# Kernel tuning notes

Measured on AMD Instinct MI355X. Metric: run time of the kernel, lower is better.

Reference implementation:

```python
import jax, jax.numpy as jnp
import numpy as np


def _build_masks():
    # pathways_mask: [G genes, P pathways], K genes per pathway (deterministic)
    G, P, K = 5000, 200, 100
    rng = np.random.default_rng(0)
    r = rng.random((G, P))
    pm = np.zeros((G, P), np.float32)
    pm[np.argpartition(r, K, axis=0)[:K], np.arange(P)[None, :]] = 1.0
    l1 = np.maximum(pm.sum(0).astype(np.int64) // 5, 4)   # divide_nodes/min_nodes defaults
    l2 = np.maximum(l1 // 2, 3)
    l3 = np.maximum(l2 // 2, 2)
    g1 = np.repeat(np.arange(P), l1)
    g2 = np.repeat(np.arange(P), l2)
    g3 = np.repeat(np.arange(P), l3)
    # masks stored transposed, [out_features, in_features], as in MaskedLinear buffer
    m1 = np.repeat(pm, l1, axis=1).T                                  # [H1, G]
    m2 = (g2[:, None] == g1[None, :]).astype(np.float32)              # [H2, H1] block-diag repeated
    m3 = (g3[:, None] == g2[None, :]).astype(np.float32)              # [H3, H2]
    m4 = (np.arange(P)[:, None] == g3[None, :]).astype(np.float32)    # [P,  H3] final_mask
    return m1, m2, m3, m4


def setup_inputs():
    B, NL = 8192, 50
    m1, m2, m3, m4 = _build_masks()
    dims = [m1.shape[1], m1.shape[0], m2.shape[0], m3.shape[0], m4.shape[0]]  # [5000,4000,2000,1000,200]
    key = jax.random.key(0)
    ks = iter(jax.random.split(key, 40))
    def W(o, i):
        return jax.random.normal(next(ks), (o, i), jnp.float32) / np.sqrt(i)
    def V(n):
        return jax.random.normal(next(ks), (n,), jnp.float32) * 0.1
    inp = {"x": jax.random.normal(next(ks), (B, dims[0]), jnp.float32)}
    for li, (i, o, m) in enumerate(zip(dims[:4], dims[1:], [m1, m2, m3, m4]), 1):
        inp[f"w{li}"] = W(o, i)
        inp[f"b{li}"] = V(o)
        inp[f"m{li}"] = jnp.asarray(m)
    for li, o in enumerate(dims[1:4], 1):
        inp[f"gamma{li}"] = 1.0 + V(o)
        inp[f"beta{li}"] = V(o)
        inp[f"rm{li}"] = V(o)
        inp[f"rv{li}"] = 0.5 + jax.random.uniform(next(ks), (o,), jnp.float32)
    inp["wc"] = W(NL, dims[4])
    inp["bc"] = V(NL)
    return inp


def _bn_relu(h, gamma, beta, rm, rv):
    # eval-mode BatchNorm1d (running stats) + ReLU; Dropout is identity at eval
    return jax.nn.relu(gamma * (h - rm) * jax.lax.rsqrt(rv + 1e-5) + beta)


def reference(x, w1, b1, m1, w2, b2, m2, w3, b3, m3, w4, b4, m4,
              gamma1, beta1, rm1, rv1, gamma2, beta2, rm2, rv2,
              gamma3, beta3, rm3, rv3, wc, bc):
    h = _bn_relu(x @ (w1 * m1).T + b1, gamma1, beta1, rm1, rv1)
    h = _bn_relu(h @ (w2 * m2).T + b2, gamma2, beta2, rm2, rv2)
    h = _bn_relu(h @ (w3 * m3).T + b3, gamma3, beta3, rm3, rv3)
    scores = jax.nn.relu(h @ (w4 * m4).T + b4)   # [B, n_pathways]
    return scores @ wc.T + bc                    # [B, n_labels]
```

## Files before the change

### kernel.cpp

```cpp
#include <hip/hip_runtime.h>
#include <hip/hip_fp16.h>
#include <stdint.h>

#define GENES 5000
#define NH1   4000
#define NH2   2000
#define NH3   1000
#define NPATH 200
#define NLAB  50
#define NROWS 8192
#define KP    100

typedef _Float16 f16x2 __attribute__((ext_vector_type(2)));
union H2U { unsigned int u; f16x2 v; __half2 h; };

__device__ __forceinline__ float dot2acc(unsigned int a, unsigned int b, float c){
#if __has_builtin(__builtin_amdgcn_fdot2)
    H2U ua; ua.u = a; H2U ub; ub.u = b;
    return __builtin_amdgcn_fdot2(ua.v, ub.v, c, false);
#else
    H2U ua; ua.u = a; H2U ub; ub.u = b;
    float2 fa = __half22float2(ua.h), fb = __half22float2(ub.h);
    return fmaf(fa.x, fb.x, fmaf(fa.y, fb.y, c));
#endif
}

__device__ __forceinline__ unsigned pklo(unsigned xa, unsigned xb){
#if __has_builtin(__builtin_amdgcn_perm)
    return __builtin_amdgcn_perm(xb, xa, 0x05040100u);
#else
    return (xa & 0xffffu) | (xb << 16);
#endif
}
__device__ __forceinline__ unsigned pkhi(unsigned xa, unsigned xb){
#if __has_builtin(__builtin_amdgcn_perm)
    return __builtin_amdgcn_perm(xb, xa, 0x07060302u);
#else
    return (xa >> 16) | (xb & 0xffff0000u);
#endif
}

__global__ void k_idx(const float* __restrict__ m1, int* __restrict__ idx1){
    __shared__ int cnt;
    if (threadIdx.x == 0) cnt = 0;
    __syncthreads();
    const float* row = m1 + (size_t)blockIdx.x * 20 * GENES;
    for (int g = threadIdx.x; g < GENES; g += blockDim.x){
        if (row[g] != 0.0f){
            int pos = atomicAdd(&cnt, 1);
            if (pos < KP) idx1[blockIdx.x * KP + pos] = g;
        }
    }
}

__global__ void k_wg1(const float* __restrict__ w1, const float* __restrict__ gamma1,
                      const float* __restrict__ rv1, const int* __restrict__ idx1,
                      __half* __restrict__ wg1p){
    int tid = blockIdx.x * 256 + threadIdx.x;
    if (tid >= 400000) return;
    int kk  = tid / 8000;
    int rem = tid % 8000;
    int c = rem >> 3;
    int e = rem & 7;
    int p = c / 5, g = c % 5;
    int u = e >> 1, kpar = e & 1;
    int k = kk * 2 + kpar;
    int j = p * 20 + g * 4 + u;
    int col = idx1[p * KP + k];
    float a = gamma1[j] * rsqrtf(rv1[j] + 1e-5f);
    wg1p[tid] = (__half)(w1[(size_t)j * GENES + col] * a);
}

__global__ void k_prep(const float* __restrict__ w2, const float* __restrict__ b2,
                       const float* __restrict__ w3, const float* __restrict__ b3,
                       const float* __restrict__ w4, const float* __restrict__ wc,
                       const float* __restrict__ gamma1, const float* __restrict__ beta1,
                       const float* __restrict__ rm1, const float* __restrict__ rv1,
                       const float* __restrict__ gamma2, const float* __restrict__ beta2,
                       const float* __restrict__ rm2, const float* __restrict__ rv2,
                       const float* __restrict__ gamma3, const float* __restrict__ beta3,
                       const float* __restrict__ rm3, const float* __restrict__ rv3,
                       const float* __restrict__ b1,
                       float* __restrict__ bf1, float* __restrict__ bf2,
                       float* __restrict__ bf3,
                       __half* __restrict__ wpk, float* __restrict__ wcT){
    int t = blockIdx.x * 256 + threadIdx.x;
    if (t < 40000){
        int p = t / 200, i = t % 200;
        int u2 = i / 20, k = i % 20;
        int j = 10 * p + u2;
        float a = gamma2[j] * rsqrtf(rv2[j] + 1e-5f);
        wpk[p * 256 + i] = (__half)(w2[(size_t)j * NH1 + 20 * p + k] * a);
    } else if (t < 50000){
        int i2 = t - 40000;
        int p = i2 / 50, i = i2 % 50;
        int u3 = i / 10, k = i % 10;
        int j = 5 * p + u3;
        float a = gamma3[j] * rsqrtf(rv3[j] + 1e-5f);
        wpk[p * 256 + 200 + i] = (__half)(w3[(size_t)j * NH2 + 10 * p + k] * a);
    } else if (t < 51000){
        int i2 = t - 50000;
        int p = i2 / 5, k = i2 % 5;
        wpk[p * 256 + 250 + k] = (__half)(w4[(size_t)p * NH3 + 5 * p + k]);
    } else if (t < 51200){
        int p = t - 51000;
        wpk[p * 256 + 255] = (__half)0.0f;
    } else if (t < 61200){
        int i = t - 51200;
        int q = i / NLAB, n = i % NLAB;
        wcT[i] = wc[(size_t)n * NPATH + q];
    } else if (t < 65200){
        int j = t - 61200;
        float a = gamma1[j] * rsqrtf(rv1[j] + 1e-5f);
        bf1[j] = a * b1[j] + beta1[j] - rm1[j] * a;
    } else if (t < 67200){
        int j = t - 65200;
        float a = gamma2[j] * rsqrtf(rv2[j] + 1e-5f);
        bf2[j] = a * b2[j] + beta2[j] - rm2[j] * a;
    } else if (t < 68200){
        int j = t - 67200;
        float a = gamma3[j] * rsqrtf(rv3[j] + 1e-5f);
        bf3[j] = a * b3[j] + beta3[j] - rm3[j] * a;
    }
}

__global__ __launch_bounds__(256) void k_layer1(const float* __restrict__ x,
        const int* __restrict__ idx1, const __half* __restrict__ wg1p,
        const float* __restrict__ bf1, __half* __restrict__ h1buf){
    __shared__ __align__(16) __half xs[GENES * 4];
    const int r0 = blockIdx.x * 4;
    for (int c = threadIdx.x; c < GENES; c += 256){
        float v0 = x[(size_t)(r0 + 0) * GENES + c];
        float v1 = x[(size_t)(r0 + 1) * GENES + c];
        float v2 = x[(size_t)(r0 + 2) * GENES + c];
        float v3 = x[(size_t)(r0 + 3) * GENES + c];
        __half2* d = (__half2*)(xs + c * 4);
        d[0] = __floats2half2_rn(v0, v1);
        d[1] = __floats2half2_rn(v2, v3);
    }
    __syncthreads();
    const int t = threadIdx.x;
    if (t >= 250) return;
    const int pl = t / 5, g = t % 5;
    for (int pass = 0; pass < 4; ++pass){
        const int p = pass * 50 + pl;
        float acc[4][4];
        #pragma unroll
        for (int u = 0; u < 4; ++u)
            #pragma unroll
            for (int r = 0; r < 4; ++r) acc[u][r] = 0.0f;
        const int2* ip = (const int2*)(idx1 + p * KP);
        const char* wb = (const char*)(((const uint4*)wg1p) + (p * 5 + g));
        int2 ivA = ip[0], ivB = ip[1];
        uint4 wvA = *(const uint4*)wb;
        uint4 wvB = *(const uint4*)(wb + 16000);
        for (int kk = 0; kk < 50; kk += 2){
            const int nk = (kk + 2 < 50) ? kk + 2 : 0;
            int2 ivA2 = ip[nk], ivB2 = ip[nk + 1];
            uint4 wvA2 = *(const uint4*)(wb + (size_t)nk * 16000);
            uint4 wvB2 = *(const uint4*)(wb + (size_t)(nk + 1) * 16000);
            {
                uint2 xa = *(const uint2*)(xs + ivA.x * 4);
                uint2 xb = *(const uint2*)(xs + ivA.y * 4);
                unsigned pr[4] = { pklo(xa.x, xb.x), pkhi(xa.x, xb.x),
                                   pklo(xa.y, xb.y), pkhi(xa.y, xb.y) };
                const unsigned wu[4] = {wvA.x, wvA.y, wvA.z, wvA.w};
                #pragma unroll
                for (int u = 0; u < 4; ++u)
                    #pragma unroll
                    for (int r = 0; r < 4; ++r)
                        acc[u][r] = dot2acc(pr[r], wu[u], acc[u][r]);
            }
            {
                uint2 xa = *(const uint2*)(xs + ivB.x * 4);
                uint2 xb = *(const uint2*)(xs + ivB.y * 4);
                unsigned pr[4] = { pklo(xa.x, xb.x), pkhi(xa.x, xb.x),
                                   pklo(xa.y, xb.y), pkhi(xa.y, xb.y) };
                const unsigned wu[4] = {wvB.x, wvB.y, wvB.z, wvB.w};
                #pragma unroll
                for (int u = 0; u < 4; ++u)
                    #pragma unroll
                    for (int r = 0; r < 4; ++r)
                        acc[u][r] = dot2acc(pr[r], wu[u], acc[u][r]);
            }
            ivA = ivA2; ivB = ivB2; wvA = wvA2; wvB = wvB2;
        }
        const float4 bf = ((const float4*)bf1)[p * 5 + g];
        const float bfa[4] = {bf.x, bf.y, bf.z, bf.w};
        const int jb = p * 20 + g * 4;
        #pragma unroll
        for (int r = 0; r < 4; ++r){
            __half2 o01 = __floats2half2_rn(fmaxf(acc[0][r] + bfa[0], 0.0f),
                                            fmaxf(acc[1][r] + bfa[1], 0.0f));
            __half2 o23 = __floats2half2_rn(fmaxf(acc[2][r] + bfa[2], 0.0f),
                                            fmaxf(acc[3][r] + bfa[3], 0.0f));
            uint2 st; st.x = *(unsigned*)&o01; st.y = *(unsigned*)&o23;
            *(uint2*)(h1buf + (size_t)(r0 + r) * NH1 + jb) = st;
        }
    }
}

__global__ __launch_bounds__(256) void k_tail(const __half* __restrict__ h1buf,
        const __half* __restrict__ wpk, const float* __restrict__ bf2,
        const float* __restrict__ bf3, const float* __restrict__ b4,
        const float* __restrict__ wcT, const float* __restrict__ bc,
        float* __restrict__ out){
    __shared__ float scs[8 * NPATH];
    __shared__ __align__(16) float wcs[NPATH * NLAB];
    const int t = threadIdx.x;
    const int r0 = blockIdx.x * 8;
    for (int i = t; i < (NPATH * NLAB) / 4; i += 256)
        ((float4*)wcs)[i] = ((const float4*)wcT)[i];
    if (t < NPATH){
        const int p = t;
        unsigned cw[128];
        const uint4* wp4 = (const uint4*)(wpk + p * 256);
        #pragma unroll
        for (int i = 0; i < 32; ++i){
            uint4 v = wp4[i];
            cw[4*i] = v.x; cw[4*i+1] = v.y; cw[4*i+2] = v.z; cw[4*i+3] = v.w;
        }
        float c2[10], c3[5];
        #pragma unroll
        for (int i = 0; i < 10; ++i) c2[i] = bf2[10 * p + i];
        #pragma unroll
        for (int i = 0; i < 5; ++i)  c3[i] = bf3[5 * p + i];
        const float b4p = b4[p];
        for (int r = 0; r < 8; ++r){
            const uint2* hp = (const uint2*)(h1buf + (size_t)(r0 + r) * NH1 + 20 * p);
            unsigned h1u[10];
            #pragma unroll
            for (int i = 0; i < 5; ++i){ uint2 v = hp[i]; h1u[2*i] = v.x; h1u[2*i+1] = v.y; }
            unsigned h2u[5];
            #pragma unroll
            for (int i = 0; i < 5; ++i){
                float a0 = c2[2*i], a1 = c2[2*i+1];
                #pragma unroll
                for (int kk = 0; kk < 10; ++kk){
                    a0 = dot2acc(h1u[kk], cw[(2*i) * 10 + kk], a0);
                    a1 = dot2acc(h1u[kk], cw[(2*i+1) * 10 + kk], a1);
                }
                __half2 hh = __floats2half2_rn(fmaxf(a0, 0.f), fmaxf(a1, 0.f));
                h2u[i] = *(unsigned*)&hh;
            }
            float h3f[5];
            #pragma unroll
            for (int u = 0; u < 5; ++u){
                float a = c3[u];
                #pragma unroll
                for (int kk = 0; kk < 5; ++kk)
                    a = dot2acc(h2u[kk], cw[100 + u * 5 + kk], a);
                h3f[u] = fmaxf(a, 0.f);
            }
            unsigned h3u[3];
            __half2 t01 = __floats2half2_rn(h3f[0], h3f[1]); h3u[0] = *(unsigned*)&t01;
            __half2 t23 = __floats2half2_rn(h3f[2], h3f[3]); h3u[1] = *(unsigned*)&t23;
            __half2 t4  = __floats2half2_rn(h3f[4], 0.f);    h3u[2] = *(unsigned*)&t4;
            float a = b4p;
            #pragma unroll
            for (int kk = 0; kk < 3; ++kk)
                a = dot2acc(h3u[kk], cw[125 + kk], a);
            scs[r * NPATH + p] = fmaxf(a, 0.f);
        }
    }
    __syncthreads();
    for (int o = t; o < 8 * NLAB; o += 256){
        int r = o / NLAB, n = o % NLAB;
        float acc = bc[n];
        const float* sp = scs + r * NPATH;
        #pragma unroll 8
        for (int q = 0; q < NPATH; ++q)
            acc = fmaf(sp[q], wcs[q * NLAB + n], acc);
        out[(size_t)(r0 + r) * NLAB + n] = acc;
    }
}

extern "C" void kernel_launch(void* const* d_in, const int* in_sizes, int n_in,
                              void* d_out, int out_size, void* d_ws, size_t ws_size,
                              hipStream_t stream){
    (void)in_sizes; (void)n_in; (void)out_size; (void)ws_size;
    const float* x      = (const float*)d_in[0];
    const float* w1     = (const float*)d_in[1];
    const float* b1     = (const float*)d_in[2];
    const float* m1     = (const float*)d_in[3];
    const float* w2     = (const float*)d_in[4];
    const float* b2     = (const float*)d_in[5];
    const float* w3     = (const float*)d_in[7];
    const float* b3     = (const float*)d_in[8];
    const float* w4     = (const float*)d_in[10];
    const float* b4     = (const float*)d_in[11];
    const float* gamma1 = (const float*)d_in[13];
    const float* beta1  = (const float*)d_in[14];
    const float* rm1    = (const float*)d_in[15];
    const float* rv1    = (const float*)d_in[16];
    const float* gamma2 = (const float*)d_in[17];
    const float* beta2  = (const float*)d_in[18];
    const float* rm2    = (const float*)d_in[19];
    const float* rv2    = (const float*)d_in[20];
    const float* gamma3 = (const float*)d_in[21];
    const float* beta3  = (const float*)d_in[22];
    const float* rm3    = (const float*)d_in[23];
    const float* rv3    = (const float*)d_in[24];
    const float* wc     = (const float*)d_in[25];
    const float* bc     = (const float*)d_in[26];

    char* ws = (char*)d_ws;
    size_t off = 0;
    __half* h1buf = (__half*)(ws + off); off += (size_t)NROWS * NH1 * 2;
    int*    idx1  = (int*)  (ws + off);  off += (size_t)NPATH * KP * 4;
    __half* wg1p  = (__half*)(ws + off); off += (size_t)400000 * 2;
    float*  bf1   = (float*)(ws + off);  off += (size_t)NH1 * 4;
    float*  bf2   = (float*)(ws + off);  off += (size_t)NH2 * 4;
    float*  bf3   = (float*)(ws + off);  off += (size_t)NH3 * 4;
    __half* wpk   = (__half*)(ws + off); off += (size_t)NPATH * 256 * 2;
    float*  wcT   = (float*)(ws + off);  off += (size_t)NPATH * NLAB * 4;

    hipLaunchKernelGGL(k_idx,    dim3(NPATH),   dim3(256), 0, stream, m1, idx1);
    hipLaunchKernelGGL(k_wg1,    dim3(1563),    dim3(256), 0, stream, w1, gamma1, rv1, idx1, wg1p);
    hipLaunchKernelGGL(k_prep,   dim3(267),     dim3(256), 0, stream,
                       w2, b2, w3, b3, w4, wc,
                       gamma1, beta1, rm1, rv1, gamma2, beta2, rm2, rv2,
                       gamma3, beta3, rm3, rv3, b1,
                       bf1, bf2, bf3, wpk, wcT);
    hipLaunchKernelGGL(k_layer1, dim3(NROWS/4), dim3(256), 0, stream, x, idx1, wg1p, bf1, h1buf);
    hipLaunchKernelGGL(k_tail,   dim3(NROWS/8), dim3(256), 0, stream,
                       h1buf, wpk, bf2, bf3, b4, wcT, bc, (float*)d_out);
}
```

Before: 538.6 us.

## Fuse layer1 and tail kernels, keep h1 in shared memory, 6 rows per block

Merges the layer-1 sparse gather kernel and the tail kernel into a single kernel that keeps the h1 activations in registers and then shared memory, so the 8192x4000 half-precision h1 buffer is never written to or read back from global memory. Each block now handles 6 rows instead of 4 and uses a deeper software-pipelined gather loop. The two weight-prep kernels are merged into one launch. The final classifier now reads wcT from global memory instead of staging it in shared memory. The trade-off is heavier register pressure (48 h1 registers plus 24 accumulators per thread), about 60KB of shared memory per block, and a row count that does not divide evenly into blocks, which adds a tail guard.

```diff
diff --git a/kernel.cpp b/kernel.cpp
--- a/kernel.cpp
+++ b/kernel.cpp
@@ -10,6 +10,7 @@
 #define NLAB  50
 #define NROWS 8192
 #define KP    100
+#define RB    6
 
 typedef _Float16 f16x2 __attribute__((ext_vector_type(2)));
 union H2U { unsigned int u; f16x2 v; __half2 h; };
@@ -53,38 +54,38 @@
     }
 }
 
-__global__ void k_wg1(const float* __restrict__ w1, const float* __restrict__ gamma1,
-                      const float* __restrict__ rv1, const int* __restrict__ idx1,
-                      __half* __restrict__ wg1p){
-    int tid = blockIdx.x * 256 + threadIdx.x;
-    if (tid >= 400000) return;
-    int kk  = tid / 8000;
-    int rem = tid % 8000;
-    int c = rem >> 3;
-    int e = rem & 7;
-    int p = c / 5, g = c % 5;
-    int u = e >> 1, kpar = e & 1;
-    int k = kk * 2 + kpar;
-    int j = p * 20 + g * 4 + u;
-    int col = idx1[p * KP + k];
-    float a = gamma1[j] * rsqrtf(rv1[j] + 1e-5f);
-    wg1p[tid] = (__half)(w1[(size_t)j * GENES + col] * a);
-}
-
-__global__ void k_prep(const float* __restrict__ w2, const float* __restrict__ b2,
-                       const float* __restrict__ w3, const float* __restrict__ b3,
-                       const float* __restrict__ w4, const float* __restrict__ wc,
-                       const float* __restrict__ gamma1, const float* __restrict__ beta1,
-                       const float* __restrict__ rm1, const float* __restrict__ rv1,
-                       const float* __restrict__ gamma2, const float* __restrict__ beta2,
-                       const float* __restrict__ rm2, const float* __restrict__ rv2,
-                       const float* __restrict__ gamma3, const float* __restrict__ beta3,
-                       const float* __restrict__ rm3, const float* __restrict__ rv3,
-                       const float* __restrict__ b1,
-                       float* __restrict__ bf1, float* __restrict__ bf2,
-                       float* __restrict__ bf3,
-                       __half* __restrict__ wpk, float* __restrict__ wcT){
-    int t = blockIdx.x * 256 + threadIdx.x;
+__global__ void k_prep2(const float* __restrict__ w1, const float* __restrict__ gamma1,
+                        const float* __restrict__ rv1, const int* __restrict__ idx1,
+                        __half* __restrict__ wg1p,
+                        const float* __restrict__ w2, const float* __restrict__ b2,
+                        const float* __restrict__ w3, const float* __restrict__ b3,
+                        const float* __restrict__ w4, const float* __restrict__ wc,
+                        const float* __restrict__ beta1, const float* __restrict__ rm1,
+                        const float* __restrict__ gamma2, const float* __restrict__ beta2,
+                        const float* __restrict__ rm2, const float* __restrict__ rv2,
+                        const float* __restrict__ gamma3, const float* __restrict__ beta3,
+                        const float* __restrict__ rm3, const float* __restrict__ rv3,
+                        const float* __restrict__ b1,
+                        float* __restrict__ bf1, float* __restrict__ bf2,
+                        float* __restrict__ bf3,
+                        __half* __restrict__ wpk, float* __restrict__ wcT){
+    if (blockIdx.x < 1563){
+        int tid = blockIdx.x * 256 + threadIdx.x;
+        if (tid >= 400000) return;
+        int kk  = tid / 8000;
+        int rem = tid % 8000;
+        int c = rem >> 3;
+        int e = rem & 7;
+        int p = c / 5, g = c % 5;
+        int u = e >> 1, kpar = e & 1;
+        int k = kk * 2 + kpar;
+        int j = p * 20 + g * 4 + u;
+        int col = idx1[p * KP + k];
+        float a = gamma1[j] * rsqrtf(rv1[j] + 1e-5f);
+        wg1p[tid] = (__half)(w1[(size_t)j * GENES + col] * a);
+        return;
+    }
+    int t = (blockIdx.x - 1563) * 256 + threadIdx.x;
     if (t < 40000){
         int p = t / 200, i = t % 200;
         int u2 = i / 20, k = i % 20;
@@ -124,93 +125,94 @@
     }
 }
 
-__global__ __launch_bounds__(256) void k_layer1(const float* __restrict__ x,
+__global__ __launch_bounds__(256, 2) void k_main(const float* __restrict__ x,
         const int* __restrict__ idx1, const __half* __restrict__ wg1p,
-        const float* __restrict__ bf1, __half* __restrict__ h1buf){
-    __shared__ __align__(16) __half xs[GENES * 4];
-    const int r0 = blockIdx.x * 4;
-    for (int c = threadIdx.x; c < GENES; c += 256){
-        float v0 = x[(size_t)(r0 + 0) * GENES + c];
-        float v1 = x[(size_t)(r0 + 1) * GENES + c];
-        float v2 = x[(size_t)(r0 + 2) * GENES + c];
-        float v3 = x[(size_t)(r0 + 3) * GENES + c];
-        __half2* d = (__half2*)(xs + c * 4);
-        d[0] = __floats2half2_rn(v0, v1);
-        d[1] = __floats2half2_rn(v2, v3);
-    }
-    __syncthreads();
-    const int t = threadIdx.x;
-    if (t >= 250) return;
-    const int pl = t / 5, g = t % 5;
-    for (int pass = 0; pass < 4; ++pass){
-        const int p = pass * 50 + pl;
-        float acc[4][4];
-        #pragma unroll
-        for (int u = 0; u < 4; ++u)
-            #pragma unroll
-            for (int r = 0; r < 4; ++r) acc[u][r] = 0.0f;
-        const int2* ip = (const int2*)(idx1 + p * KP);
-        const char* wb = (const char*)(((const uint4*)wg1p) + (p * 5 + g));
-        int2 ivA = ip[0], ivB = ip[1];
-        uint4 wvA = *(const uint4*)wb;
-        uint4 wvB = *(const uint4*)(wb + 16000);
-        for (int kk = 0; kk < 50; kk += 2){
-            const int nk = (kk + 2 < 50) ? kk + 2 : 0;
-            int2 ivA2 = ip[nk], ivB2 = ip[nk + 1];
-            uint4 wvA2 = *(const uint4*)(wb + (size_t)nk * 16000);
-            uint4 wvB2 = *(const uint4*)(wb + (size_t)(nk + 1) * 16000);
-            {
-                uint2 xa = *(const uint2*)(xs + ivA.x * 4);
-                uint2 xb = *(const uint2*)(xs + ivA.y * 4);
-                unsigned pr[4] = { pklo(xa.x, xb.x), pkhi(xa.x, xb.x),
-                                   pklo(xa.y, xb.y), pkhi(xa.y, xb.y) };
-                const unsigned wu[4] = {wvA.x, wvA.y, wvA.z, wvA.w};
-                #pragma unroll
-                for (int u = 0; u < 4; ++u)
-                    #pragma unroll
-                    for (int r = 0; r < 4; ++r)
-                        acc[u][r] = dot2acc(pr[r], wu[u], acc[u][r]);
-            }
-            {
-                uint2 xa = *(const uint2*)(xs + ivB.x * 4);
-                uint2 xb = *(const uint2*)(xs + ivB.y * 4);
-                unsigned pr[4] = { pklo(xa.x, xb.x), pkhi(xa.x, xb.x),
-                                   pklo(xa.y, xb.y), pkhi(xa.y, xb.y) };
-                const unsigned wu[4] = {wvB.x, wvB.y, wvB.z, wvB.w};
-                #pragma unroll
-                for (int u = 0; u < 4; ++u)
-                    #pragma unroll
-                    for (int r = 0; r < 4; ++r)
-                        acc[u][r] = dot2acc(pr[r], wu[u], acc[u][r]);
-            }
-            ivA = ivA2; ivB = ivB2; wvA = wvA2; wvB = wvB2;
-        }
-        const float4 bf = ((const float4*)bf1)[p * 5 + g];
-        const float bfa[4] = {bf.x, bf.y, bf.z, bf.w};
-        const int jb = p * 20 + g * 4;
-        #pragma unroll
-        for (int r = 0; r < 4; ++r){
-            __half2 o01 = __floats2half2_rn(fmaxf(acc[0][r] + bfa[0], 0.0f),
-                                            fmaxf(acc[1][r] + bfa[1], 0.0f));
-            __half2 o23 = __floats2half2_rn(fmaxf(acc[2][r] + bfa[2], 0.0f),
-                                            fmaxf(acc[3][r] + bfa[3], 0.0f));
-            uint2 st; st.x = *(unsigned*)&o01; st.y = *(unsigned*)&o23;
-            *(uint2*)(h1buf + (size_t)(r0 + r) * NH1 + jb) = st;
-        }
-    }
-}
-
-__global__ __launch_bounds__(256) void k_tail(const __half* __restrict__ h1buf,
+        const float* __restrict__ bf1,
         const __half* __restrict__ wpk, const float* __restrict__ bf2,
         const float* __restrict__ bf3, const float* __restrict__ b4,
         const float* __restrict__ wcT, const float* __restrict__ bc,
         float* __restrict__ out){
-    __shared__ float scs[8 * NPATH];
-    __shared__ __align__(16) float wcs[NPATH * NLAB];
+    __shared__ __align__(16) unsigned char smem[60000];
+    __shared__ float scs[RB * NPATH];
     const int t = threadIdx.x;
-    const int r0 = blockIdx.x * 8;
-    for (int i = t; i < (NPATH * NLAB) / 4; i += 256)
-        ((float4*)wcs)[i] = ((const float4*)wcT)[i];
+    const int r0 = blockIdx.x * RB;
+    const int rvld = min(RB, NROWS - r0);
+
+    for (int c = t; c < GENES; c += 256){
+        float v[RB];
+        #pragma unroll
+        for (int r = 0; r < RB; ++r)
+            v[r] = (r < rvld) ? x[(size_t)(r0 + r) * GENES + c] : 0.0f;
+        unsigned* d = (unsigned*)(smem + c * 12);
+        __half2 h01 = __floats2half2_rn(v[0], v[1]);
+        __half2 h23 = __floats2half2_rn(v[2], v[3]);
+        __half2 h45 = __floats2half2_rn(v[4], v[5]);
+        d[0] = *(unsigned*)&h01; d[1] = *(unsigned*)&h23; d[2] = *(unsigned*)&h45;
+    }
+    __syncthreads();
+
+    unsigned h1r[48];
+    const int pl = t / 5, g = t % 5;
+    if (t < 250){
+        #pragma unroll 1
+        for (int pass = 0; pass < 4; ++pass){
+            const int p = pass * 50 + pl;
+            const int2* ip = (const int2*)(idx1 + p * KP);
+            const uint4* wp = ((const uint4*)wg1p) + (p * 5 + g);
+            float acc[4][RB];
+            #pragma unroll
+            for (int u = 0; u < 4; ++u)
+                #pragma unroll
+                for (int r = 0; r < RB; ++r) acc[u][r] = 0.0f;
+            int2 iv0 = ip[0], iv1 = ip[1], iv2 = ip[2];
+            uint4 wv0 = wp[0], wv1 = wp[1000], wv2 = wp[2000];
+            uint3 xa0 = *(const uint3*)(smem + iv0.x * 12);
+            uint3 xb0 = *(const uint3*)(smem + iv0.y * 12);
+            for (int kk = 0; kk < 50; ++kk){
+                int nk = kk + 3; nk = (nk > 49) ? 49 : nk;
+                int2 ivN = ip[nk];
+                uint4 wvN = wp[(size_t)nk * 1000];
+                uint3 xa1 = *(const uint3*)(smem + iv1.x * 12);
+                uint3 xb1 = *(const uint3*)(smem + iv1.y * 12);
+                unsigned pr[RB] = { pklo(xa0.x, xb0.x), pkhi(xa0.x, xb0.x),
+                                    pklo(xa0.y, xb0.y), pkhi(xa0.y, xb0.y),
+                                    pklo(xa0.z, xb0.z), pkhi(xa0.z, xb0.z) };
+                const unsigned wu[4] = {wv0.x, wv0.y, wv0.z, wv0.w};
+                #pragma unroll
+                for (int u = 0; u < 4; ++u)
+                    #pragma unroll
+                    for (int r = 0; r < RB; ++r)
+                        acc[u][r] = dot2acc(pr[r], wu[u], acc[u][r]);
+                iv0 = iv1; iv1 = iv2; iv2 = ivN;
+                wv0 = wv1; wv1 = wv2; wv2 = wvN;
+                xa0 = xa1; xb0 = xb1;
+            }
+            const float4 bf = ((const float4*)bf1)[p * 5 + g];
+            #pragma unroll
+            for (int r = 0; r < RB; ++r){
+                __half2 o01 = __floats2half2_rn(fmaxf(acc[0][r] + bf.x, 0.0f),
+                                                fmaxf(acc[1][r] + bf.y, 0.0f));
+                __half2 o23 = __floats2half2_rn(fmaxf(acc[2][r] + bf.z, 0.0f),
+                                                fmaxf(acc[3][r] + bf.w, 0.0f));
+                h1r[pass * 12 + r * 2]     = *(unsigned*)&o01;
+                h1r[pass * 12 + r * 2 + 1] = *(unsigned*)&o23;
+            }
+        }
+    }
+    __syncthreads();
+    if (t < 250){
+        #pragma unroll 1
+        for (int pass = 0; pass < 4; ++pass){
+            const int j0 = (pass * 50 + pl) * 20 + g * 4;
+            #pragma unroll
+            for (int r = 0; r < RB; ++r){
+                uint2 st; st.x = h1r[pass * 12 + r * 2]; st.y = h1r[pass * 12 + r * 2 + 1];
+                *(uint2*)(smem + r * 8000 + j0 * 2) = st;
+            }
+        }
+    }
+    __syncthreads();
+
     if (t < NPATH){
         const int p = t;
         unsigned cw[128];
@@ -226,8 +228,8 @@
         #pragma unroll
         for (int i = 0; i < 5; ++i)  c3[i] = bf3[5 * p + i];
         const float b4p = b4[p];
-        for (int r = 0; r < 8; ++r){
-            const uint2* hp = (const uint2*)(h1buf + (size_t)(r0 + r) * NH1 + 20 * p);
+        for (int r = 0; r < RB; ++r){
+            const uint2* hp = (const uint2*)(smem + r * 8000 + p * 40);
             unsigned h1u[10];
             #pragma unroll
             for (int i = 0; i < 5; ++i){ uint2 v = hp[i]; h1u[2*i] = v.x; h1u[2*i+1] = v.y; }
@@ -264,14 +266,17 @@
         }
     }
     __syncthreads();
-    for (int o = t; o < 8 * NLAB; o += 256){
+
+    for (int o = t; o < RB * NLAB; o += 256){
         int r = o / NLAB, n = o % NLAB;
-        float acc = bc[n];
-        const float* sp = scs + r * NPATH;
-        #pragma unroll 8
-        for (int q = 0; q < NPATH; ++q)
-            acc = fmaf(sp[q], wcs[q * NLAB + n], acc);
-        out[(size_t)(r0 + r) * NLAB + n] = acc;
+        if (r0 + r < NROWS){
+            float acc2 = bc[n];
+            const float* sp = scs + r * NPATH;
+            #pragma unroll 8
+            for (int q = 0; q < NPATH; ++q)
+                acc2 = fmaf(sp[q], wcT[q * NLAB + n], acc2);
+            out[(size_t)(r0 + r) * NLAB + n] = acc2;
+        }
     }
 }
 
@@ -306,7 +311,6 @@
 
     char* ws = (char*)d_ws;
     size_t off = 0;
-    __half* h1buf = (__half*)(ws + off); off += (size_t)NROWS * NH1 * 2;
     int*    idx1  = (int*)  (ws + off);  off += (size_t)NPATH * KP * 4;
     __half* wg1p  = (__half*)(ws + off); off += (size_t)400000 * 2;
     float*  bf1   = (float*)(ws + off);  off += (size_t)NH1 * 4;
@@ -315,14 +319,14 @@
     __half* wpk   = (__half*)(ws + off); off += (size_t)NPATH * 256 * 2;
     float*  wcT   = (float*)(ws + off);  off += (size_t)NPATH * NLAB * 4;
 
-    hipLaunchKernelGGL(k_idx,    dim3(NPATH),   dim3(256), 0, stream, m1, idx1);
-    hipLaunchKernelGGL(k_wg1,    dim3(1563),    dim3(256), 0, stream, w1, gamma1, rv1, idx1, wg1p);
-    hipLaunchKernelGGL(k_prep,   dim3(267),     dim3(256), 0, stream,
+    const int nblk = (NROWS + RB - 1) / RB;
+    hipLaunchKernelGGL(k_idx,   dim3(NPATH),  dim3(256), 0, stream, m1, idx1);
+    hipLaunchKernelGGL(k_prep2, dim3(1830),   dim3(256), 0, stream,
+                       w1, gamma1, rv1, idx1, wg1p,
                        w2, b2, w3, b3, w4, wc,
-                       gamma1, beta1, rm1, rv1, gamma2, beta2, rm2, rv2,
+                       beta1, rm1, gamma2, beta2, rm2, rv2,
                        gamma3, beta3, rm3, rv3, b1,
                        bf1, bf2, bf3, wpk, wcT);
-    hipLaunchKernelGGL(k_layer1, dim3(NROWS/4), dim3(256), 0, stream, x, idx1, wg1p, bf1, h1buf);
-    hipLaunchKernelGGL(k_tail,   dim3(NROWS/8), dim3(256), 0, stream,
-                       h1buf, wpk, bf2, bf3, b4, wcT, bc, (float*)d_out);
-}
+    hipLaunchKernelGGL(k_main,  dim3(nblk),   dim3(256), 0, stream,
+                       x, idx1, wg1p, bf1, wpk, bf2, bf3, b4, wcT, bc, (float*)d_out);
+}
```

New measurement: 779.8 us. 44.8% more time.
